# Performance work log

Hardware: AMD Instinct MI355X
Metric: run time of the kernel (lower is better)

Reference implementation:

```python
import jax, jax.numpy as jnp
import numpy as np

A = 32      # num_agents (nodes per batch element)
B = 256     # batch size
T = 5       # temporal_window_size
H, C = 4, 64  # attention heads, hidden_dim per head
D = H * C   # feature_dim = 256
NEG_SLOPE = 0.2
LATENT = 128
NBS = 64    # num_belief_states
FIN = NBS + 16  # node_feat_dim = num_belief_states + action_dim


def _xavier(k, shape):
    std = (2.0 / (shape[0] + shape[-1])) ** 0.5
    return std * jax.random.normal(k, shape, dtype=jnp.float32)


def setup_inputs() -> dict:
    key = jax.random.key(0)
    ks = jax.random.split(key, 24)
    N = B * A
    # fully-connected directed graph (no self loops) inside each batch block
    ii, jj = np.meshgrid(np.arange(A), np.arange(A), indexing='ij')
    m = ii != jj
    off = (np.arange(B) * A)[:, None]
    src = (off + ii[m][None, :]).ravel()
    dst = (off + jj[m][None, :]).ravel()
    edge_index = jnp.asarray(np.stack([src, dst]), dtype=jnp.int32)  # [2, E]
    return dict(
        x_seq=jax.random.normal(ks[0], (T, N, FIN), dtype=jnp.float32),
        edge_index=edge_index,
        W1=_xavier(ks[1], (D, FIN)),
        att_src1=0.1 * jax.random.normal(ks[2], (H, C), dtype=jnp.float32),
        att_dst1=0.1 * jax.random.normal(ks[3], (H, C), dtype=jnp.float32),
        b1=jnp.zeros((D,), jnp.float32),
        W2=_xavier(ks[4], (D, D)),
        att_src2=0.1 * jax.random.normal(ks[5], (H, C), dtype=jnp.float32),
        att_dst2=0.1 * jax.random.normal(ks[6], (H, C), dtype=jnp.float32),
        b2=jnp.zeros((D,), jnp.float32),
        in_proj_w=_xavier(ks[7], (3 * D, D)),
        in_proj_b=jnp.zeros((3 * D,), jnp.float32),
        out_proj_w=_xavier(ks[8], (D, D)),
        out_proj_b=jnp.zeros((D,), jnp.float32),
        w_mean=_xavier(ks[9], (LATENT, D)),
        b_mean=jnp.zeros((LATENT,), jnp.float32),
        w_logvar=_xavier(ks[10], (LATENT, D)),
        b_logvar=jnp.zeros((LATENT,), jnp.float32),
        w_belief=_xavier(ks[11], (NBS, D)),
        b_belief=jnp.zeros((NBS,), jnp.float32),
    )


def _gat(x, src, dst, W, a_src, a_dst, bias, N):
    """PyG-style GATConv (concat heads, self loops already in src/dst, eval mode)."""
    h = (x @ W.T).reshape(N, H, C)                         # [N,H,C]
    e = (h * a_src).sum(-1)[src] + (h * a_dst).sum(-1)[dst]  # [E,H]
    e = jax.nn.leaky_relu(e, NEG_SLOPE)
    mx = jax.ops.segment_max(e, dst, num_segments=N)       # segment softmax over incoming edges
    ex = jnp.exp(e - mx[dst])
    denom = jax.ops.segment_sum(ex, dst, num_segments=N)
    alpha = ex / denom[dst]                                # [E,H]
    out = jax.ops.segment_sum(h[src] * alpha[:, :, None], dst, num_segments=N)
    return out.reshape(N, H * C) + bias


def reference(x_seq, edge_index, W1, att_src1, att_dst1, b1, W2, att_src2, att_dst2, b2,
              in_proj_w, in_proj_b, out_proj_w, out_proj_b,
              w_mean, b_mean, w_logvar, b_logvar, w_belief, b_belief):
    N = x_seq.shape[1]
    loops = jnp.arange(N, dtype=edge_index.dtype)          # GATConv adds self loops
    src = jnp.concatenate([edge_index[0], loops])
    dst = jnp.concatenate([edge_index[1], loops])
    ego = jnp.arange(0, N, A)                              # ego node of each batch element

    def step(_, x):
        hh = jax.nn.relu(_gat(x, src, dst, W1, att_src1, att_dst1, b1, N))
        hh = jax.nn.relu(_gat(hh, src, dst, W2, att_src2, att_dst2, b2, N))
        return None, hh[ego]                               # [B, D]

    _, outs = jax.lax.scan(step, None, x_seq)              # [T, B, D]
    seq = jnp.transpose(outs, (1, 0, 2))                   # [B, T, D]

    # nn.MultiheadAttention(batch_first=True), float additive mask of 1s (j<=i) / 0s (j>i)
    qkv = seq @ in_proj_w.T + in_proj_b
    q, k, v = jnp.split(qkv, 3, axis=-1)
    split = lambda t: t.reshape(B, T, H, D // H).transpose(0, 2, 1, 3)  # [B,H,T,dh]
    q, k, v = split(q), split(k), split(v)
    mask = (jnp.arange(T)[:, None] >= jnp.arange(T)[None, :]).astype(seq.dtype)
    scale = 1.0 / jnp.sqrt(jnp.asarray(D // H, seq.dtype))
    scores = jnp.einsum('bhqd,bhkd->bhqk', q, k) * scale + mask
    attn = jax.nn.softmax(scores, axis=-1)
    ctx = jnp.einsum('bhqk,bhkd->bhqd', attn, v).transpose(0, 2, 1, 3).reshape(B, T, D)
    attn_out = ctx @ out_proj_w.T + out_proj_b
    feat = attn_out[:, -1]                                 # [B, D]

    mean = feat @ w_mean.T + b_mean
    logvar = feat @ w_logvar.T + b_logvar
    belief = jax.nn.softmax(feat @ w_belief.T + b_belief, axis=-1)
    return mean, logvar, belief
```

## Files before the change

### kernel.cpp

```cpp
#include <hip/hip_runtime.h>

typedef _Float16 f16;
typedef __attribute__((ext_vector_type(2))) _Float16 f16x2;
typedef __attribute__((ext_vector_type(4))) _Float16 f16x4;
typedef __attribute__((ext_vector_type(8))) _Float16 f16x8;
typedef __attribute__((ext_vector_type(4))) float    f32x4;

#define NA 32
#define NB 256
#define NT 5
#define ND 256
#define NFIN 80
#define NLAT 128
#define NBEL 64
#define NEG 0.2f

#define W1K 96
#define XSTR 104
#define H1TSTR 40
#define HH1STR 264
#define ALSTR 40

#define OFF_XS  0
#define OFF_ALP 6656
#define OFF_HH1 0
#define OFF_H1T 16896
#define OFF_SD  37376
#define SMEM_SZ 38400

#define MFMA16(a,b,c) __builtin_amdgcn_mfma_f32_16x16x32_f16(a, b, c, 0, 0, 0)

#define WS_SEQ   0
#define WS_QKV   655360
#define WS_Z2    655360
#define WS_CTX   2621440
#define WS_W1F   2752512
#define WS_W2F   2801664
#define WS_IPW   2932736
#define WS_OPW   3325952
#define WS_HDW   3457024
#define WS_WSD1  3620864
#define WS_WSD2  3623936

__global__ void convert_w(const float* __restrict__ W1, const float* __restrict__ W2,
                          const float* __restrict__ ipw, const float* __restrict__ opw,
                          const float* __restrict__ wm, const float* __restrict__ wl,
                          const float* __restrict__ wb,
                          const float* __restrict__ as1, const float* __restrict__ ad1,
                          const float* __restrict__ as2, const float* __restrict__ ad2,
                          f16* __restrict__ W1f, f16* __restrict__ W2f,
                          f16* __restrict__ ipwf, f16* __restrict__ opwf,
                          f16* __restrict__ hdwf,
                          f16* __restrict__ wsd1f, f16* __restrict__ wsd2f)
{
    const int i = blockIdx.x * 256 + threadIdx.x;
    if (i < 24576) {
        const int r = i / W1K, c = i - r * W1K;
        W1f[i] = (c < NFIN) ? (f16)W1[r * NFIN + c] : (f16)0.f;
    } else if (i < 90112) {
        const int j = i - 24576; W2f[j] = (f16)W2[j];
    } else if (i < 286720) {
        const int j = i - 90112; ipwf[j] = (f16)ipw[j];
    } else if (i < 352256) {
        const int j = i - 286720; opwf[j] = (f16)opw[j];
    } else if (i < 434176) {
        const int j = i - 352256;
        hdwf[j] = (f16)(j < 32768 ? wm[j] : (j < 65536 ? wl[j - 32768] : wb[j - 65536]));
    } else if (i < 435712) {
        const int j = i - 434176;
        const int o = j / 96, f = j - o * 96;
        float v = 0.f;
        if (o < 8 && f < NFIN) {
            const int h = o & 3;
            const float* av = (o < 4) ? as1 : ad1;
            for (int cc = 0; cc < 64; ++cc)
                v = fmaf(av[h * 64 + cc], W1[(h * 64 + cc) * NFIN + f], v);
        }
        wsd1f[j] = (f16)v;
    } else if (i < 439808) {
        const int j = i - 435712;
        const int o = j >> 8, k = j & 255;
        float v = 0.f;
        if (o < 8) {
            const int h = o & 3;
            const float* av = (o < 4) ? as2 : ad2;
            for (int cc = 0; cc < 64; ++cc)
                v = fmaf(av[h * 64 + cc], W2[(h * 64 + cc) * ND + k], v);
        }
        wsd2f[j] = (f16)v;
    }
}

__global__ __launch_bounds__(256, 2)
void gnn_kernel(const float* __restrict__ x_seq,
                const f16*  __restrict__ W1f,  const f16* __restrict__ wsd1f,
                const float* __restrict__ b1,
                const f16*  __restrict__ wsd2f,
                f16* __restrict__ z2g)
{
    __shared__ __align__(16) unsigned char smem[SMEM_SZ];
    f16*  Xs  = (f16*)(smem + OFF_XS);
    f16*  hh1 = (f16*)(smem + OFF_HH1);
    f16*  alp = (f16*)(smem + OFF_ALP);
    f16*  h1T = (f16*)(smem + OFF_H1T);
    float* sA = (float*)(smem + OFF_SD);
    float* dA = sA + 128;

    const int blk  = blockIdx.x;
    const int b    = blk / NT;
    const int t    = blk % NT;
    const int tid  = threadIdx.x;
    const int wv   = tid >> 6;
    const int lane = tid & 63;
    const int c    = lane & 15;
    const int g    = lane >> 4;
    const int n0   = wv * 64;
    const int kg   = 8 * g;

    f16x8 w1s[3], w1b[3][4];
#pragma unroll
    for (int kt = 0; kt < 3; ++kt) {
        const int k0 = kt * 32 + kg;
        w1s[kt] = *(const f16x8*)(wsd1f + c * W1K + k0);
#pragma unroll
        for (int tn = 0; tn < 4; ++tn)
            w1b[kt][tn] = *(const f16x8*)(W1f + (size_t)(n0 + 16 * tn + c) * W1K + k0);
    }

    const float* xg = x_seq + ((size_t)t * (NB * NA) + (size_t)b * NA) * NFIN;
    for (int idx = tid; idx < 640; idx += 256) {
        const int r = idx / 20, c4 = idx - r * 20;
        const float4 v = ((const float4*)xg)[idx];
        f16x4 h; h.x = (f16)v.x; h.y = (f16)v.y; h.z = (f16)v.z; h.w = (f16)v.w;
        *(f16x4*)(Xs + r * XSTR + c4 * 4) = h;
    }
    if (tid < 128) {
        const int r = tid >> 2, cc = tid & 3;
        f16x4 z; z.x = z.y = z.z = z.w = (f16)0.f;
        *(f16x4*)(Xs + r * XSTR + 80 + cc * 4) = z;
    }
    __syncthreads();

    f32x4 acc1[2][4]; f32x4 accS[2];
#pragma unroll
    for (int m = 0; m < 2; ++m) {
        accS[m] = (f32x4)0.f;
#pragma unroll
        for (int tn = 0; tn < 4; ++tn) acc1[m][tn] = (f32x4)0.f;
    }
#pragma unroll
    for (int kt = 0; kt < 3; ++kt) {
        const int k0 = kt * 32 + kg;
        f16x8 a0 = *(const f16x8*)(Xs + c * XSTR + k0);
        f16x8 a1 = *(const f16x8*)(Xs + (16 + c) * XSTR + k0);
        accS[0] = MFMA16(a0, w1s[kt], accS[0]);
        accS[1] = MFMA16(a1, w1s[kt], accS[1]);
#pragma unroll
        for (int tn = 0; tn < 4; ++tn) {
            acc1[0][tn] = MFMA16(a0, w1b[kt][tn], acc1[0][tn]);
            acc1[1][tn] = MFMA16(a1, w1b[kt][tn], acc1[1][tn]);
        }
    }

    if (c == wv) {
#pragma unroll
        for (int m = 0; m < 2; ++m)
#pragma unroll
            for (int r = 0; r < 4; ++r)
                sA[wv * 32 + 16 * m + 4 * g + r] = accS[m][r];
    } else if (c == wv + 4) {
#pragma unroll
        for (int m = 0; m < 2; ++m)
#pragma unroll
            for (int r = 0; r < 4; ++r)
                dA[wv * 32 + 16 * m + 4 * g + r] = accS[m][r];
    }

#pragma unroll
    for (int m = 0; m < 2; ++m)
#pragma unroll
        for (int tn = 0; tn < 4; ++tn) {
            f16x4 h;
            h.x = (f16)acc1[m][tn][0]; h.y = (f16)acc1[m][tn][1];
            h.z = (f16)acc1[m][tn][2]; h.w = (f16)acc1[m][tn][3];
            *(f16x4*)(h1T + (n0 + 16 * tn + c) * H1TSTR + 16 * m + 4 * g) = h;
        }

    {
        const int j = lane & 31;
        const int half = lane >> 5;
        const float dd = dA[wv * 32 + j];
        const float* sbase = sA + wv * 32 + 16 * half;
        float e[16]; float mx = -1e30f;
#pragma unroll
        for (int i = 0; i < 16; ++i) {
            float v = sbase[i] + dd;
            v = (v >= 0.f) ? v : NEG * v;
            e[i] = v; mx = fmaxf(mx, v);
        }
        mx = fmaxf(mx, __shfl_xor(mx, 32, 64));
        float den = 0.f;
#pragma unroll
        for (int i = 0; i < 16; ++i) { float p = __expf(e[i] - mx); e[i] = p; den += p; }
        den += __shfl_xor(den, 32, 64);
        const float rr = 1.f / den;
        f16* arow = alp + (wv * 32 + j) * ALSTR + 16 * half;
#pragma unroll
        for (int i2 = 0; i2 < 8; ++i2) {
            f16x2 p2; p2.x = (f16)(e[2 * i2] * rr); p2.y = (f16)(e[2 * i2 + 1] * rr);
            *(f16x2*)(arow + 2 * i2) = p2;
        }
    }

    f32x4 accT[4][2];
#pragma unroll
    for (int mt = 0; mt < 4; ++mt)
#pragma unroll
        for (int jt = 0; jt < 2; ++jt) accT[mt][jt] = (f32x4)0.f;
    {
        f16x8 bal0 = *(const f16x8*)(alp + (wv * 32 + c) * ALSTR + kg);
        f16x8 bal1 = *(const f16x8*)(alp + (wv * 32 + 16 + c) * ALSTR + kg);
#pragma unroll
        for (int mt = 0; mt < 4; ++mt) {
            f16x8 ah = *(const f16x8*)(h1T + (n0 + 16 * mt + c) * H1TSTR + kg);
            accT[mt][0] = MFMA16(ah, bal0, accT[mt][0]);
            accT[mt][1] = MFMA16(ah, bal1, accT[mt][1]);
        }
    }

    __syncthreads();

    f32x4 bqa[4];
#pragma unroll
    for (int mt = 0; mt < 4; ++mt)
        bqa[mt] = *(const f32x4*)&b1[n0 + 16 * mt + 4 * g];
#pragma unroll
    for (int mt = 0; mt < 4; ++mt) {
#pragma unroll
        for (int jt = 0; jt < 2; ++jt) {
            f16x4 h;
            h.x = (f16)fmaxf(accT[mt][jt][0] + bqa[mt][0], 0.f);
            h.y = (f16)fmaxf(accT[mt][jt][1] + bqa[mt][1], 0.f);
            h.z = (f16)fmaxf(accT[mt][jt][2] + bqa[mt][2], 0.f);
            h.w = (f16)fmaxf(accT[mt][jt][3] + bqa[mt][3], 0.f);
            *(f16x4*)(hh1 + (16 * jt + c) * HH1STR + n0 + 16 * mt + 4 * g) = h;
        }
    }
    __syncthreads();

    f16x8 w2s[8];
#pragma unroll
    for (int kt = 0; kt < 8; ++kt)
        w2s[kt] = *(const f16x8*)(wsd2f + c * ND + kt * 32 + kg);

    f32x4 accS2[2];
    accS2[0] = (f32x4)0.f; accS2[1] = (f32x4)0.f;
#pragma unroll
    for (int kt = 0; kt < 8; ++kt) {
        const int k0 = kt * 32 + kg;
        f16x8 a0 = *(const f16x8*)(hh1 + c * HH1STR + k0);
        f16x8 a1 = *(const f16x8*)(hh1 + (16 + c) * HH1STR + k0);
        accS2[0] = MFMA16(a0, w2s[kt], accS2[0]);
        accS2[1] = MFMA16(a1, w2s[kt], accS2[1]);
    }

    if (c == wv) {
#pragma unroll
        for (int m = 0; m < 2; ++m)
#pragma unroll
            for (int r = 0; r < 4; ++r)
                sA[wv * 32 + 16 * m + 4 * g + r] = accS2[m][r];
    }
    if (c == wv + 4 && g == 0) dA[wv * 32] = accS2[0][0];

    const float d20 = dA[wv * 32];

    {
        float mx = -1e30f;
#pragma unroll
        for (int i = 0; i < 32; ++i) {
            float v = sA[wv * 32 + i] + d20;
            v = (v >= 0.f) ? v : NEG * v;
            mx = fmaxf(mx, v);
        }
        float den = 0.f;
#pragma unroll
        for (int i = 0; i < 32; ++i) {
            float v = sA[wv * 32 + i] + d20;
            v = (v >= 0.f) ? v : NEG * v;
            den += __expf(v - mx);
        }
        float e0, e1;
        {
            float v = sA[wv * 32 + c] + d20;
            v = (v >= 0.f) ? v : NEG * v;
            e0 = __expf(v - mx);
        }
        {
            float v = sA[wv * 32 + 16 + c] + d20;
            v = (v >= 0.f) ? v : NEG * v;
            e1 = __expf(v - mx);
        }
        const float rden = 1.f / den;
        f16* zo = z2g + (size_t)blk * ND;
#pragma unroll
        for (int mt = 0; mt < 4; ++mt) {
            f32x4 zv;
#pragma unroll
            for (int r = 0; r < 4; ++r) {
                const float h0 = fmaxf(accT[mt][0][r] + bqa[mt][r], 0.f);
                const float h1v = fmaxf(accT[mt][1][r] + bqa[mt][r], 0.f);
                zv[r] = e0 * h0 + e1 * h1v;
            }
#pragma unroll
            for (int r = 0; r < 4; ++r) {
                zv[r] += __shfl_xor(zv[r], 1, 64);
                zv[r] += __shfl_xor(zv[r], 2, 64);
                zv[r] += __shfl_xor(zv[r], 4, 64);
                zv[r] += __shfl_xor(zv[r], 8, 64);
            }
            if (c == 0) {
                f16x4 h;
                h.x = (f16)(zv[0] * rden); h.y = (f16)(zv[1] * rden);
                h.z = (f16)(zv[2] * rden); h.w = (f16)(zv[3] * rden);
                *(f16x4*)(zo + n0 + 16 * mt + 4 * g) = h;
            }
        }
    }
}

#define QASTR 264
__global__ __launch_bounds__(256, 4)
void seq_kernel(const f16* __restrict__ z2g, const f16* __restrict__ W2f,
                const float* __restrict__ b2, f16* __restrict__ seqf)
{
    __shared__ __align__(16) f16 As[64 * QASTR];

    const int bx  = blockIdx.x;
    const int m0  = (bx % 20) * 64;
    const int n0  = (bx / 20) * 128;
    const int tid = threadIdx.x;
    const int wv  = tid >> 6;
    const int lane = tid & 63;
    const int c   = lane & 15;
    const int g   = lane >> 4;
    const int mb  = (wv >> 1) * 32;
    const int nb  = n0 + (wv & 1) * 64;

    for (int idx = tid; idx < 2048; idx += 256) {
        const int r = idx >> 5, c8 = idx & 31;
        *(f16x8*)(As + r * QASTR + c8 * 8) =
            *(const f16x8*)(z2g + (size_t)(m0 + r) * ND + c8 * 8);
    }
    __syncthreads();

    f32x4 acc[2][4];
#pragma unroll
    for (int m = 0; m < 2; ++m)
#pragma unroll
        for (int tn = 0; tn < 4; ++tn) acc[m][tn] = (f32x4)0.f;

#pragma unroll
    for (int kt = 0; kt < 8; ++kt) {
        const int k0 = kt * 32 + 8 * g;
        f16x8 a0 = *(const f16x8*)(As + (mb + c) * QASTR + k0);
        f16x8 a1 = *(const f16x8*)(As + (mb + 16 + c) * QASTR + k0);
#pragma unroll
        for (int tn = 0; tn < 4; ++tn) {
            f16x8 bw = *(const f16x8*)(W2f + (size_t)(nb + 16 * tn + c) * ND + k0);
            acc[0][tn] = MFMA16(a0, bw, acc[0][tn]);
            acc[1][tn] = MFMA16(a1, bw, acc[1][tn]);
        }
    }

    float bias[4];
#pragma unroll
    for (int tn = 0; tn < 4; ++tn) bias[tn] = b2[nb + 16 * tn + c];
#pragma unroll
    for (int m = 0; m < 2; ++m)
#pragma unroll
        for (int tn = 0; tn < 4; ++tn)
#pragma unroll
            for (int r = 0; r < 4; ++r) {
                const int row = m0 + mb + 16 * m + 4 * g + r;
                seqf[(size_t)row * ND + nb + 16 * tn + c] =
                    (f16)fmaxf(acc[m][tn][r] + bias[tn], 0.f);
            }
}

__global__ __launch_bounds__(256, 4)
void qkv_kernel(const f16* __restrict__ seqf, const f16* __restrict__ ipwf,
                const float* __restrict__ ipb, f16* __restrict__ qkv)
{
    __shared__ __align__(16) f16 As[64 * QASTR];

    const int bx  = blockIdx.x;
    const int m0  = (bx % 20) * 64;
    const int n0  = (bx / 20) * 128;
    const int tid = threadIdx.x;
    const int wv  = tid >> 6;
    const int lane = tid & 63;
    const int c   = lane & 15;
    const int g   = lane >> 4;
    const int mb  = (wv >> 1) * 32;
    const int nb  = n0 + (wv & 1) * 64;

    for (int idx = tid; idx < 2048; idx += 256) {
        const int r = idx >> 5, c8 = idx & 31;
        *(f16x8*)(As + r * QASTR + c8 * 8) =
            *(const f16x8*)(seqf + (size_t)(m0 + r) * ND + c8 * 8);
    }
    __syncthreads();

    f32x4 acc[2][4];
#pragma unroll
    for (int m = 0; m < 2; ++m)
#pragma unroll
        for (int tn = 0; tn < 4; ++tn) acc[m][tn] = (f32x4)0.f;

#pragma unroll
    for (int kt = 0; kt < 8; ++kt) {
        const int k0 = kt * 32 + 8 * g;
        f16x8 a0 = *(const f16x8*)(As + (mb + c) * QASTR + k0);
        f16x8 a1 = *(const f16x8*)(As + (mb + 16 + c) * QASTR + k0);
#pragma unroll
        for (int tn = 0; tn < 4; ++tn) {
            f16x8 bw = *(const f16x8*)(ipwf + (size_t)(nb + 16 * tn + c) * ND + k0);
            acc[0][tn] = MFMA16(a0, bw, acc[0][tn]);
            acc[1][tn] = MFMA16(a1, bw, acc[1][tn]);
        }
    }

    float bias[4];
#pragma unroll
    for (int tn = 0; tn < 4; ++tn) bias[tn] = ipb[nb + 16 * tn + c];
#pragma unroll
    for (int m = 0; m < 2; ++m)
#pragma unroll
        for (int tn = 0; tn < 4; ++tn)
#pragma unroll
            for (int r = 0; r < 4; ++r) {
                const int row = m0 + mb + 16 * m + 4 * g + r;
                qkv[(size_t)row * 768 + nb + 16 * tn + c] =
                    (f16)(acc[m][tn][r] + bias[tn]);
            }
}

__global__ __launch_bounds__(256, 4)
void attn_kernel(const f16* __restrict__ qkv, f16* __restrict__ ctx)
{
    const int b    = blockIdx.x;
    const int wv   = threadIdx.x >> 6;
    const int lane = threadIdx.x & 63;
    const int ch   = wv * 64 + lane;

    const float q = (float)qkv[(size_t)(b * 5 + 4) * 768 + ch];
    float kv[NT], vv[NT];
#pragma unroll
    for (int t = 0; t < NT; ++t) {
        kv[t] = (float)qkv[(size_t)(b * 5 + t) * 768 + 256 + ch];
        vv[t] = (float)qkv[(size_t)(b * 5 + t) * 768 + 512 + ch];
    }
    float sc[NT];
#pragma unroll
    for (int t = 0; t < NT; ++t) {
        float p = q * kv[t];
#pragma unroll
        for (int off = 32; off > 0; off >>= 1) p += __shfl_xor(p, off, 64);
        sc[t] = p * 0.125f;
    }
    float m = sc[0];
#pragma unroll
    for (int t = 1; t < NT; ++t) m = fmaxf(m, sc[t]);
    float den = 0.f, o = 0.f;
#pragma unroll
    for (int t = 0; t < NT; ++t) {
        float p = __expf(sc[t] - m);
        den += p;
        o = fmaf(p, vv[t], o);
    }
    ctx[(size_t)b * ND + ch] = (f16)(o / den);
}

#define FASTR 264
__global__ __launch_bounds__(256, 2)
void final_kernel(const f16* __restrict__ ctx,
                  const f16* __restrict__ opwf, const float* __restrict__ opb,
                  const f16* __restrict__ hdwf,
                  const float* __restrict__ bm, const float* __restrict__ blv,
                  const float* __restrict__ bb,
                  float* __restrict__ out)
{
    __shared__ __align__(16) f16 As[32 * FASTR];
    __shared__ __align__(16) f16 Fs[32 * FASTR];
    __shared__ __align__(16) float Bs[32 * 68];

    const int m0   = blockIdx.x * 32;
    const int tid  = threadIdx.x;
    const int wv   = tid >> 6;
    const int lane = tid & 63;
    const int c    = lane & 15;
    const int g    = lane >> 4;

    for (int idx = tid; idx < 1024; idx += 256) {
        const int r = idx >> 5, c8 = idx & 31;
        *(f16x8*)(As + r * FASTR + c8 * 8) =
            *(const f16x8*)(ctx + (size_t)(m0 + r) * ND + c8 * 8);
    }
    __syncthreads();

    {
        f32x4 acc[2][4];
#pragma unroll
        for (int m = 0; m < 2; ++m)
#pragma unroll
            for (int tn = 0; tn < 4; ++tn) acc[m][tn] = (f32x4)0.f;
#pragma unroll
        for (int kt = 0; kt < 8; ++kt) {
            const int k0 = kt * 32 + 8 * g;
            f16x8 a0 = *(const f16x8*)(As + c * FASTR + k0);
            f16x8 a1 = *(const f16x8*)(As + (16 + c) * FASTR + k0);
#pragma unroll
            for (int tn = 0; tn < 4; ++tn) {
                f16x8 bw = *(const f16x8*)(opwf + (size_t)(wv * 64 + 16 * tn + c) * ND + k0);
                acc[0][tn] = MFMA16(a0, bw, acc[0][tn]);
                acc[1][tn] = MFMA16(a1, bw, acc[1][tn]);
            }
        }
        float bias[4];
#pragma unroll
        for (int tn = 0; tn < 4; ++tn) bias[tn] = opb[wv * 64 + 16 * tn + c];
#pragma unroll
        for (int m = 0; m < 2; ++m)
#pragma unroll
            for (int tn = 0; tn < 4; ++tn)
#pragma unroll
                for (int r = 0; r < 4; ++r)
                    Fs[(16 * m + 4 * g + r) * FASTR + wv * 64 + 16 * tn + c] =
                        (f16)(acc[m][tn][r] + bias[tn]);
    }
    __syncthreads();

    {
        f32x4 acc[2][5];
#pragma unroll
        for (int m = 0; m < 2; ++m)
#pragma unroll
            for (int fi = 0; fi < 5; ++fi) acc[m][fi] = (f32x4)0.f;
#pragma unroll
        for (int kt = 0; kt < 8; ++kt) {
            const int k0 = kt * 32 + 8 * g;
            f16x8 a0 = *(const f16x8*)(Fs + c * FASTR + k0);
            f16x8 a1 = *(const f16x8*)(Fs + (16 + c) * FASTR + k0);
#pragma unroll
            for (int fi = 0; fi < 5; ++fi) {
                const int nf = 5 * wv + fi;
                f16x8 bw = *(const f16x8*)(hdwf + (size_t)(16 * nf + c) * ND + k0);
                acc[0][fi] = MFMA16(a0, bw, acc[0][fi]);
                acc[1][fi] = MFMA16(a1, bw, acc[1][fi]);
            }
        }
#pragma unroll
        for (int fi = 0; fi < 5; ++fi) {
            const int ocol = 16 * (5 * wv + fi) + c;
            float bias;
            if (ocol < 128)       bias = bm[ocol];
            else if (ocol < 256)  bias = blv[ocol - 128];
            else                  bias = bb[ocol - 256];
#pragma unroll
            for (int m = 0; m < 2; ++m)
#pragma unroll
                for (int r = 0; r < 4; ++r) {
                    const int row = 16 * m + 4 * g + r;
                    const float v = acc[m][fi][r] + bias;
                    if (ocol < 128)
                        out[(size_t)(m0 + row) * NLAT + ocol] = v;
                    else if (ocol < 256)
                        out[(size_t)NB * NLAT + (size_t)(m0 + row) * NLAT + (ocol - 128)] = v;
                    else
                        Bs[row * 68 + (ocol - 256)] = v;
                }
        }
    }
    __syncthreads();

    for (int rr = 0; rr < 8; ++rr) {
        const int row = wv * 8 + rr;
        float x = Bs[row * 68 + lane];
        float mm = x;
#pragma unroll
        for (int off = 32; off > 0; off >>= 1) mm = fmaxf(mm, __shfl_xor(mm, off, 64));
        float p = __expf(x - mm);
        float dd = p;
#pragma unroll
        for (int off = 32; off > 0; off >>= 1) dd += __shfl_xor(dd, off, 64);
        out[(size_t)2 * NB * NLAT + (size_t)(m0 + row) * NBEL + lane] = p / dd;
    }
}

extern "C" void kernel_launch(void* const* d_in, const int* in_sizes, int n_in,
                              void* d_out, int out_size, void* d_ws, size_t ws_size,
                              hipStream_t stream)
{
    (void)in_sizes; (void)n_in; (void)out_size; (void)ws_size;
    const float* x_seq = (const float*)d_in[0];
    const float* W1  = (const float*)d_in[2];
    const float* as1 = (const float*)d_in[3];
    const float* ad1 = (const float*)d_in[4];
    const float* b1  = (const float*)d_in[5];
    const float* W2  = (const float*)d_in[6];
    const float* as2 = (const float*)d_in[7];
    const float* ad2 = (const float*)d_in[8];
    const float* b2  = (const float*)d_in[9];
    const float* ipw = (const float*)d_in[10];
    const float* ipb = (const float*)d_in[11];
    const float* opw = (const float*)d_in[12];
    const float* opb = (const float*)d_in[13];
    const float* wm  = (const float*)d_in[14];
    const float* bm  = (const float*)d_in[15];
    const float* wl  = (const float*)d_in[16];
    const float* bl  = (const float*)d_in[17];
    const float* wb  = (const float*)d_in[18];
    const float* bb  = (const float*)d_in[19];

    char* ws = (char*)d_ws;
    f16* seqf  = (f16*)(ws + WS_SEQ);
    f16* qkv   = (f16*)(ws + WS_QKV);
    f16* z2g   = (f16*)(ws + WS_Z2);
    f16* ctx   = (f16*)(ws + WS_CTX);
    f16* W1f   = (f16*)(ws + WS_W1F);
    f16* W2f   = (f16*)(ws + WS_W2F);
    f16* ipwf  = (f16*)(ws + WS_IPW);
    f16* opwf  = (f16*)(ws + WS_OPW);
    f16* hdwf  = (f16*)(ws + WS_HDW);
    f16* wsd1f = (f16*)(ws + WS_WSD1);
    f16* wsd2f = (f16*)(ws + WS_WSD2);
    float* out = (float*)d_out;

    hipLaunchKernelGGL(convert_w, dim3(1718), dim3(256), 0, stream,
                       W1, W2, ipw, opw, wm, wl, wb, as1, ad1, as2, ad2,
                       W1f, W2f, ipwf, opwf, hdwf, wsd1f, wsd2f);
    hipLaunchKernelGGL(gnn_kernel, dim3(NB * NT), dim3(256), 0, stream,
                       x_seq, W1f, wsd1f, b1, wsd2f, z2g);
    hipLaunchKernelGGL(seq_kernel, dim3(40), dim3(256), 0, stream,
                       z2g, W2f, b2, seqf);
    hipLaunchKernelGGL(qkv_kernel, dim3(120), dim3(256), 0, stream,
                       seqf, ipwf, ipb, qkv);
    hipLaunchKernelGGL(attn_kernel, dim3(NB), dim3(256), 0, stream, qkv, ctx);
    hipLaunchKernelGGL(final_kernel, dim3(8), dim3(256), 0, stream,
                       ctx, opwf, opb, hdwf, bm, bl, bb, out);
}
```

Baseline: 62.16 us.

## Process two graph blocks per GNN workgroup with prefetched inputs and shuffle softmax

The GNN kernel now runs 640 workgroups, and each handles two (batch, time) graphs: blk0 and blk0+640, which maps to batch b+128. Both graphs' inputs are prefetched into registers up front, and the W1 register fragments are reused across the two graphs. The second-layer softmax now uses wave shuffles across 32 values instead of each lane serially looping over all 32 entries in LDS. The aim is to amortize weight loads and launch overhead and hide global load latency, in exchange for higher register pressure and less parallelism across the grid.

```diff
diff --git a/kernel.cpp b/kernel.cpp
--- a/kernel.cpp
+++ b/kernel.cpp
@@ -106,9 +106,9 @@
     float* sA = (float*)(smem + OFF_SD);
     float* dA = sA + 128;
 
-    const int blk  = blockIdx.x;
-    const int b    = blk / NT;
-    const int t    = blk % NT;
+    const int blk0 = blockIdx.x;
+    const int b    = blk0 / NT;
+    const int t    = blk0 % NT;
     const int tid  = threadIdx.x;
     const int wv   = tid >> 6;
     const int lane = tid & 63;
@@ -127,203 +127,219 @@
             w1b[kt][tn] = *(const f16x8*)(W1f + (size_t)(n0 + 16 * tn + c) * W1K + k0);
     }
 
-    const float* xg = x_seq + ((size_t)t * (NB * NA) + (size_t)b * NA) * NFIN;
-    for (int idx = tid; idx < 640; idx += 256) {
-        const int r = idx / 20, c4 = idx - r * 20;
-        const float4 v = ((const float4*)xg)[idx];
-        f16x4 h; h.x = (f16)v.x; h.y = (f16)v.y; h.z = (f16)v.z; h.w = (f16)v.w;
-        *(f16x4*)(Xs + r * XSTR + c4 * 4) = h;
-    }
+    const float* xg0 = x_seq + ((size_t)t * (NB * NA) + (size_t)b * NA) * NFIN;
+    const float* xg1 = xg0 + (size_t)128 * NA * NFIN;
+    float4 px[2][3];
+    px[0][0] = ((const float4*)xg0)[tid];
+    px[0][1] = ((const float4*)xg0)[tid + 256];
+    px[1][0] = ((const float4*)xg1)[tid];
+    px[1][1] = ((const float4*)xg1)[tid + 256];
     if (tid < 128) {
-        const int r = tid >> 2, cc = tid & 3;
-        f16x4 z; z.x = z.y = z.z = z.w = (f16)0.f;
-        *(f16x4*)(Xs + r * XSTR + 80 + cc * 4) = z;
-    }
-    __syncthreads();
-
-    f32x4 acc1[2][4]; f32x4 accS[2];
-#pragma unroll
-    for (int m = 0; m < 2; ++m) {
-        accS[m] = (f32x4)0.f;
-#pragma unroll
-        for (int tn = 0; tn < 4; ++tn) acc1[m][tn] = (f32x4)0.f;
-    }
-#pragma unroll
-    for (int kt = 0; kt < 3; ++kt) {
-        const int k0 = kt * 32 + kg;
-        f16x8 a0 = *(const f16x8*)(Xs + c * XSTR + k0);
-        f16x8 a1 = *(const f16x8*)(Xs + (16 + c) * XSTR + k0);
-        accS[0] = MFMA16(a0, w1s[kt], accS[0]);
-        accS[1] = MFMA16(a1, w1s[kt], accS[1]);
-#pragma unroll
-        for (int tn = 0; tn < 4; ++tn) {
-            acc1[0][tn] = MFMA16(a0, w1b[kt][tn], acc1[0][tn]);
-            acc1[1][tn] = MFMA16(a1, w1b[kt][tn], acc1[1][tn]);
-        }
-    }
-
-    if (c == wv) {
+        px[0][2] = ((const float4*)xg0)[tid + 512];
+        px[1][2] = ((const float4*)xg1)[tid + 512];
+    }
+
+#pragma unroll
+    for (int it = 0; it < 2; ++it) {
+        if (it) __syncthreads();
+
+        {
+            const int r0 = tid / 20,        c40 = tid - r0 * 20;
+            const int r1 = (tid + 256) / 20, c41 = (tid + 256) - r1 * 20;
+            float4 v = px[it][0];
+            f16x4 h; h.x = (f16)v.x; h.y = (f16)v.y; h.z = (f16)v.z; h.w = (f16)v.w;
+            *(f16x4*)(Xs + r0 * XSTR + c40 * 4) = h;
+            v = px[it][1];
+            h.x = (f16)v.x; h.y = (f16)v.y; h.z = (f16)v.z; h.w = (f16)v.w;
+            *(f16x4*)(Xs + r1 * XSTR + c41 * 4) = h;
+            if (tid < 128) {
+                const int r2 = (tid + 512) / 20, c42 = (tid + 512) - r2 * 20;
+                v = px[it][2];
+                h.x = (f16)v.x; h.y = (f16)v.y; h.z = (f16)v.z; h.w = (f16)v.w;
+                *(f16x4*)(Xs + r2 * XSTR + c42 * 4) = h;
+                const int rp = tid >> 2, cp = tid & 3;
+                f16x4 z; z.x = z.y = z.z = z.w = (f16)0.f;
+                *(f16x4*)(Xs + rp * XSTR + 80 + cp * 4) = z;
+            }
+        }
+        __syncthreads();
+
+        f32x4 acc1[2][4]; f32x4 accS[2];
+#pragma unroll
+        for (int m = 0; m < 2; ++m) {
+            accS[m] = (f32x4)0.f;
+#pragma unroll
+            for (int tn = 0; tn < 4; ++tn) acc1[m][tn] = (f32x4)0.f;
+        }
+#pragma unroll
+        for (int kt = 0; kt < 3; ++kt) {
+            const int k0 = kt * 32 + kg;
+            f16x8 a0 = *(const f16x8*)(Xs + c * XSTR + k0);
+            f16x8 a1 = *(const f16x8*)(Xs + (16 + c) * XSTR + k0);
+            accS[0] = MFMA16(a0, w1s[kt], accS[0]);
+            accS[1] = MFMA16(a1, w1s[kt], accS[1]);
+#pragma unroll
+            for (int tn = 0; tn < 4; ++tn) {
+                acc1[0][tn] = MFMA16(a0, w1b[kt][tn], acc1[0][tn]);
+                acc1[1][tn] = MFMA16(a1, w1b[kt][tn], acc1[1][tn]);
+            }
+        }
+
+        if (c == wv) {
+#pragma unroll
+            for (int m = 0; m < 2; ++m)
+#pragma unroll
+                for (int r = 0; r < 4; ++r)
+                    sA[wv * 32 + 16 * m + 4 * g + r] = accS[m][r];
+        } else if (c == wv + 4) {
+#pragma unroll
+            for (int m = 0; m < 2; ++m)
+#pragma unroll
+                for (int r = 0; r < 4; ++r)
+                    dA[wv * 32 + 16 * m + 4 * g + r] = accS[m][r];
+        }
+
 #pragma unroll
         for (int m = 0; m < 2; ++m)
 #pragma unroll
-            for (int r = 0; r < 4; ++r)
-                sA[wv * 32 + 16 * m + 4 * g + r] = accS[m][r];
-    } else if (c == wv + 4) {
-#pragma unroll
-        for (int m = 0; m < 2; ++m)
-#pragma unroll
-            for (int r = 0; r < 4; ++r)
-                dA[wv * 32 + 16 * m + 4 * g + r] = accS[m][r];
-    }
-
-#pragma unroll
-    for (int m = 0; m < 2; ++m)
-#pragma unroll
-        for (int tn = 0; tn < 4; ++tn) {
-            f16x4 h;
-            h.x = (f16)acc1[m][tn][0]; h.y = (f16)acc1[m][tn][1];
-            h.z = (f16)acc1[m][tn][2]; h.w = (f16)acc1[m][tn][3];
-            *(f16x4*)(h1T + (n0 + 16 * tn + c) * H1TSTR + 16 * m + 4 * g) = h;
-        }
-
-    {
-        const int j = lane & 31;
-        const int half = lane >> 5;
-        const float dd = dA[wv * 32 + j];
-        const float* sbase = sA + wv * 32 + 16 * half;
-        float e[16]; float mx = -1e30f;
-#pragma unroll
-        for (int i = 0; i < 16; ++i) {
-            float v = sbase[i] + dd;
-            v = (v >= 0.f) ? v : NEG * v;
-            e[i] = v; mx = fmaxf(mx, v);
-        }
-        mx = fmaxf(mx, __shfl_xor(mx, 32, 64));
-        float den = 0.f;
-#pragma unroll
-        for (int i = 0; i < 16; ++i) { float p = __expf(e[i] - mx); e[i] = p; den += p; }
-        den += __shfl_xor(den, 32, 64);
-        const float rr = 1.f / den;
-        f16* arow = alp + (wv * 32 + j) * ALSTR + 16 * half;
-#pragma unroll
-        for (int i2 = 0; i2 < 8; ++i2) {
-            f16x2 p2; p2.x = (f16)(e[2 * i2] * rr); p2.y = (f16)(e[2 * i2 + 1] * rr);
-            *(f16x2*)(arow + 2 * i2) = p2;
-        }
-    }
-
-    f32x4 accT[4][2];
-#pragma unroll
-    for (int mt = 0; mt < 4; ++mt)
-#pragma unroll
-        for (int jt = 0; jt < 2; ++jt) accT[mt][jt] = (f32x4)0.f;
-    {
-        f16x8 bal0 = *(const f16x8*)(alp + (wv * 32 + c) * ALSTR + kg);
-        f16x8 bal1 = *(const f16x8*)(alp + (wv * 32 + 16 + c) * ALSTR + kg);
+            for (int tn = 0; tn < 4; ++tn) {
+                f16x4 h;
+                h.x = (f16)acc1[m][tn][0]; h.y = (f16)acc1[m][tn][1];
+                h.z = (f16)acc1[m][tn][2]; h.w = (f16)acc1[m][tn][3];
+                *(f16x4*)(h1T + (n0 + 16 * tn + c) * H1TSTR + 16 * m + 4 * g) = h;
+            }
+
+        {
+            const int j = lane & 31;
+            const int half = lane >> 5;
+            const float dd = dA[wv * 32 + j];
+            const float* sbase = sA + wv * 32 + 16 * half;
+            float e[16]; float mx = -1e30f;
+#pragma unroll
+            for (int i = 0; i < 16; ++i) {
+                float v = sbase[i] + dd;
+                v = (v >= 0.f) ? v : NEG * v;
+                e[i] = v; mx = fmaxf(mx, v);
+            }
+            mx = fmaxf(mx, __shfl_xor(mx, 32, 64));
+            float den = 0.f;
+#pragma unroll
+            for (int i = 0; i < 16; ++i) { float p = __expf(e[i] - mx); e[i] = p; den += p; }
+            den += __shfl_xor(den, 32, 64);
+            const float rr = 1.f / den;
+            f16* arow = alp + (wv * 32 + j) * ALSTR + 16 * half;
+#pragma unroll
+            for (int i2 = 0; i2 < 8; ++i2) {
+                f16x2 p2; p2.x = (f16)(e[2 * i2] * rr); p2.y = (f16)(e[2 * i2 + 1] * rr);
+                *(f16x2*)(arow + 2 * i2) = p2;
+            }
+        }
+
+        f32x4 accT[4][2];
+#pragma unroll
+        for (int mt = 0; mt < 4; ++mt)
+#pragma unroll
+            for (int jt = 0; jt < 2; ++jt) accT[mt][jt] = (f32x4)0.f;
+        {
+            f16x8 bal0 = *(const f16x8*)(alp + (wv * 32 + c) * ALSTR + kg);
+            f16x8 bal1 = *(const f16x8*)(alp + (wv * 32 + 16 + c) * ALSTR + kg);
+#pragma unroll
+            for (int mt = 0; mt < 4; ++mt) {
+                f16x8 ah = *(const f16x8*)(h1T + (n0 + 16 * mt + c) * H1TSTR + kg);
+                accT[mt][0] = MFMA16(ah, bal0, accT[mt][0]);
+                accT[mt][1] = MFMA16(ah, bal1, accT[mt][1]);
+            }
+        }
+
+        __syncthreads();
+
+        f32x4 bqa[4];
+#pragma unroll
+        for (int mt = 0; mt < 4; ++mt)
+            bqa[mt] = *(const f32x4*)&b1[n0 + 16 * mt + 4 * g];
 #pragma unroll
         for (int mt = 0; mt < 4; ++mt) {
-            f16x8 ah = *(const f16x8*)(h1T + (n0 + 16 * mt + c) * H1TSTR + kg);
-            accT[mt][0] = MFMA16(ah, bal0, accT[mt][0]);
-            accT[mt][1] = MFMA16(ah, bal1, accT[mt][1]);
-        }
-    }
-
-    __syncthreads();
-
-    f32x4 bqa[4];
-#pragma unroll
-    for (int mt = 0; mt < 4; ++mt)
-        bqa[mt] = *(const f32x4*)&b1[n0 + 16 * mt + 4 * g];
-#pragma unroll
-    for (int mt = 0; mt < 4; ++mt) {
-#pragma unroll
-        for (int jt = 0; jt < 2; ++jt) {
-            f16x4 h;
-            h.x = (f16)fmaxf(accT[mt][jt][0] + bqa[mt][0], 0.f);
-            h.y = (f16)fmaxf(accT[mt][jt][1] + bqa[mt][1], 0.f);
-            h.z = (f16)fmaxf(accT[mt][jt][2] + bqa[mt][2], 0.f);
-            h.w = (f16)fmaxf(accT[mt][jt][3] + bqa[mt][3], 0.f);
-            *(f16x4*)(hh1 + (16 * jt + c) * HH1STR + n0 + 16 * mt + 4 * g) = h;
-        }
-    }
-    __syncthreads();
-
-    f16x8 w2s[8];
-#pragma unroll
-    for (int kt = 0; kt < 8; ++kt)
-        w2s[kt] = *(const f16x8*)(wsd2f + c * ND + kt * 32 + kg);
-
-    f32x4 accS2[2];
-    accS2[0] = (f32x4)0.f; accS2[1] = (f32x4)0.f;
-#pragma unroll
-    for (int kt = 0; kt < 8; ++kt) {
-        const int k0 = kt * 32 + kg;
-        f16x8 a0 = *(const f16x8*)(hh1 + c * HH1STR + k0);
-        f16x8 a1 = *(const f16x8*)(hh1 + (16 + c) * HH1STR + k0);
-        accS2[0] = MFMA16(a0, w2s[kt], accS2[0]);
-        accS2[1] = MFMA16(a1, w2s[kt], accS2[1]);
-    }
-
-    if (c == wv) {
-#pragma unroll
-        for (int m = 0; m < 2; ++m)
-#pragma unroll
-            for (int r = 0; r < 4; ++r)
-                sA[wv * 32 + 16 * m + 4 * g + r] = accS2[m][r];
-    }
-    if (c == wv + 4 && g == 0) dA[wv * 32] = accS2[0][0];
-
-    const float d20 = dA[wv * 32];
-
-    {
-        float mx = -1e30f;
-#pragma unroll
-        for (int i = 0; i < 32; ++i) {
-            float v = sA[wv * 32 + i] + d20;
-            v = (v >= 0.f) ? v : NEG * v;
-            mx = fmaxf(mx, v);
-        }
-        float den = 0.f;
-#pragma unroll
-        for (int i = 0; i < 32; ++i) {
-            float v = sA[wv * 32 + i] + d20;
-            v = (v >= 0.f) ? v : NEG * v;
-            den += __expf(v - mx);
-        }
-        float e0, e1;
+#pragma unroll
+            for (int jt = 0; jt < 2; ++jt) {
+                f16x4 h;
+                h.x = (f16)fmaxf(accT[mt][jt][0] + bqa[mt][0], 0.f);
+                h.y = (f16)fmaxf(accT[mt][jt][1] + bqa[mt][1], 0.f);
+                h.z = (f16)fmaxf(accT[mt][jt][2] + bqa[mt][2], 0.f);
+                h.w = (f16)fmaxf(accT[mt][jt][3] + bqa[mt][3], 0.f);
+                *(f16x4*)(hh1 + (16 * jt + c) * HH1STR + n0 + 16 * mt + 4 * g) = h;
+            }
+        }
+        __syncthreads();
+
+        f16x8 w2s[8];
+#pragma unroll
+        for (int kt = 0; kt < 8; ++kt)
+            w2s[kt] = *(const f16x8*)(wsd2f + c * ND + kt * 32 + kg);
+
+        f32x4 accS2[2];
+        accS2[0] = (f32x4)0.f; accS2[1] = (f32x4)0.f;
+#pragma unroll
+        for (int kt = 0; kt < 8; ++kt) {
+            const int k0 = kt * 32 + kg;
+            f16x8 a0 = *(const f16x8*)(hh1 + c * HH1STR + k0);
+            f16x8 a1 = *(const f16x8*)(hh1 + (16 + c) * HH1STR + k0);
+            accS2[0] = MFMA16(a0, w2s[kt], accS2[0]);
+            accS2[1] = MFMA16(a1, w2s[kt], accS2[1]);
+        }
+
+        if (c == wv) {
+#pragma unroll
+            for (int m = 0; m < 2; ++m)
+#pragma unroll
+                for (int r = 0; r < 4; ++r)
+                    sA[wv * 32 + 16 * m + 4 * g + r] = accS2[m][r];
+        }
+        if (c == wv + 4 && g == 0) dA[wv * 32] = accS2[0][0];
+
+        const float d20 = dA[wv * 32];
+
         {
-            float v = sA[wv * 32 + c] + d20;
-            v = (v >= 0.f) ? v : NEG * v;
-            e0 = __expf(v - mx);
-        }
-        {
-            float v = sA[wv * 32 + 16 + c] + d20;
-            v = (v >= 0.f) ? v : NEG * v;
-            e1 = __expf(v - mx);
-        }
-        const float rden = 1.f / den;
-        f16* zo = z2g + (size_t)blk * ND;
-#pragma unroll
-        for (int mt = 0; mt < 4; ++mt) {
-            f32x4 zv;
-#pragma unroll
-            for (int r = 0; r < 4; ++r) {
-                const float h0 = fmaxf(accT[mt][0][r] + bqa[mt][r], 0.f);
-                const float h1v = fmaxf(accT[mt][1][r] + bqa[mt][r], 0.f);
-                zv[r] = e0 * h0 + e1 * h1v;
-            }
-#pragma unroll
-            for (int r = 0; r < 4; ++r) {
-                zv[r] += __shfl_xor(zv[r], 1, 64);
-                zv[r] += __shfl_xor(zv[r], 2, 64);
-                zv[r] += __shfl_xor(zv[r], 4, 64);
-                zv[r] += __shfl_xor(zv[r], 8, 64);
-            }
-            if (c == 0) {
-                f16x4 h;
-                h.x = (f16)(zv[0] * rden); h.y = (f16)(zv[1] * rden);
-                h.z = (f16)(zv[2] * rden); h.w = (f16)(zv[3] * rden);
-                *(f16x4*)(zo + n0 + 16 * mt + 4 * g) = h;
+            float v0 = sA[wv * 32 + c] + d20;
+            v0 = (v0 >= 0.f) ? v0 : NEG * v0;
+            float v1 = sA[wv * 32 + 16 + c] + d20;
+            v1 = (v1 >= 0.f) ? v1 : NEG * v1;
+            float mx = fmaxf(v0, v1);
+            mx = fmaxf(mx, __shfl_xor(mx, 1, 64));
+            mx = fmaxf(mx, __shfl_xor(mx, 2, 64));
+            mx = fmaxf(mx, __shfl_xor(mx, 4, 64));
+            mx = fmaxf(mx, __shfl_xor(mx, 8, 64));
+            const float e0 = __expf(v0 - mx);
+            const float e1 = __expf(v1 - mx);
+            float den = e0 + e1;
+            den += __shfl_xor(den, 1, 64);
+            den += __shfl_xor(den, 2, 64);
+            den += __shfl_xor(den, 4, 64);
+            den += __shfl_xor(den, 8, 64);
+            const float rden = 1.f / den;
+
+            f16* zo = z2g + (size_t)(blk0 + it * 640) * ND;
+#pragma unroll
+            for (int mt = 0; mt < 4; ++mt) {
+                f32x4 zv;
+#pragma unroll
+                for (int r = 0; r < 4; ++r) {
+                    const float h0 = fmaxf(accT[mt][0][r] + bqa[mt][r], 0.f);
+                    const float h1v = fmaxf(accT[mt][1][r] + bqa[mt][r], 0.f);
+                    zv[r] = e0 * h0 + e1 * h1v;
+                }
+#pragma unroll
+                for (int r = 0; r < 4; ++r) {
+                    zv[r] += __shfl_xor(zv[r], 1, 64);
+                    zv[r] += __shfl_xor(zv[r], 2, 64);
+                    zv[r] += __shfl_xor(zv[r], 4, 64);
+                    zv[r] += __shfl_xor(zv[r], 8, 64);
+                }
+                if (c == 0) {
+                    f16x4 h;
+                    h.x = (f16)(zv[0] * rden); h.y = (f16)(zv[1] * rden);
+                    h.z = (f16)(zv[2] * rden); h.w = (f16)(zv[3] * rden);
+                    *(f16x4*)(zo + n0 + 16 * mt + 4 * g) = h;
+                }
             }
         }
     }
@@ -640,7 +656,7 @@
     hipLaunchKernelGGL(convert_w, dim3(1718), dim3(256), 0, stream,
                        W1, W2, ipw, opw, wm, wl, wb, as1, ad1, as2, ad2,
                        W1f, W2f, ipwf, opwf, hdwf, wsd1f, wsd2f);
-    hipLaunchKernelGGL(gnn_kernel, dim3(NB * NT), dim3(256), 0, stream,
+    hipLaunchKernelGGL(gnn_kernel, dim3(640), dim3(256), 0, stream,
                        x_seq, W1f, wsd1f, b1, wsd2f, z2g);
     hipLaunchKernelGGL(seq_kernel, dim3(40), dim3(256), 0, stream,
                        z2g, W2f, b2, seqf);
```

Result: slower. 66.14 us (+6.4%).
